# Optimization experiments

Measured on AMD Instinct MI355X. Metric: run time of the kernel, lower is better.

## Reference

```python
import jax, jax.numpy as jnp
import numpy as np

S, B, D, H = 512, 256, 256, 256  # seq, batch, input_dim, hidden_dim
E = D + H                        # attention embed dim


def setup_inputs() -> dict:
    key = jax.random.key(0)
    ks = jax.random.split(key, 9)
    w = lambda k, shape: (jax.random.normal(k, shape, jnp.float32) * 0.02)
    return {
        "inputs": jax.random.normal(ks[0], (S, B, D), jnp.float32),
        "Wq": w(ks[1], (E, E)),
        "Wk": w(ks[2], (E, E)),
        "Wv": w(ks[3], (E, E)),
        "Wf": w(ks[4], (H, E)), "bf": jnp.zeros((H,), jnp.float32),
        "Wi": w(ks[5], (H, E)), "bi": jnp.zeros((H,), jnp.float32),
        "Wg": w(ks[6], (H, E)), "bg": jnp.zeros((H,), jnp.float32),
        "Wo": w(ks[7], (H, E)), "bo": jnp.zeros((H,), jnp.float32),
    }


def reference(inputs, Wq, Wk, Wv, Wf, bf, Wi, bi, Wg, bg, Wo, bo):
    seq, batch, d_in = inputs.shape
    h_dim = Wf.shape[0]
    scale = 1.0 / np.sqrt(d_in + h_dim)

    def step(carry, x):
        hx, cx = carry
        comb = jnp.concatenate([x, hx], axis=1)            # (B, E)
        q = comb @ Wq.T
        k = comb @ Wk.T
        v = comb @ Wv.T
        # NOTE: attention is over the batch dimension, as in the source.
        scores = jax.nn.softmax((q @ k.T) * scale, axis=-1)  # (B, B)
        attn = scores @ v                                    # (B, E)
        f = jax.nn.sigmoid(attn @ Wf.T + bf)
        i = jax.nn.sigmoid(attn @ Wi.T + bi)
        g = jnp.tanh(attn @ Wg.T + bg)
        o = jax.nn.sigmoid(attn @ Wo.T + bo)
        cx_new = f * cx + i * g
        hx_new = o * jnp.tanh(cx_new)
        return (hx_new, cx_new), hx_new

    init = (jnp.zeros((batch, h_dim), inputs.dtype),
            jnp.zeros((batch, h_dim), inputs.dtype))
    (hx, cx), stacked = jax.lax.scan(step, init, inputs)
    return stacked, (hx, cx)
```

## Files before the change

### kernel.cpp

```cpp
#include <hip/hip_runtime.h>
#include <hip/hip_bf16.h>


typedef __hip_bfloat16 bf16;
typedef __attribute__((ext_vector_type(8))) short bf16x8;
typedef __attribute__((ext_vector_type(4))) float f32x4;
typedef unsigned long long u64;

#define SEQ 512
#define NSTEP 8
#define BB  256
#define DD  256
#define HH  256
#define EE  512
#define NWG 64
#define QK_SCALE 0.04419417382415922f

#define WS_COMB0  0
#define WS_COMB1  262144
#define WS_COMBT0 524288
#define WS_COMBT1 786432
#define WS_CX     1048576
#define WS_MT     1310720
#define WS_UF     1835008
#define WS_UI     2097152
#define WS_UG     2359296
#define WS_UO     2621440
#define WS_FLAGS  2883584
#define WS_REL    2887680
#define WS_END    2888192

__device__ __forceinline__ float sigm(float x) { return 1.0f / (1.0f + __expf(-x)); }

__device__ __forceinline__ unsigned short f2bf_s(float f) {
  bf16 h = __float2bfloat16(f);
  return *reinterpret_cast<unsigned short*>(&h);
}
__device__ __forceinline__ u64 pack4(float a, float b, float c, float d) {
  union { unsigned short s[4]; u64 u; } x;
  x.s[0] = f2bf_s(a); x.s[1] = f2bf_s(b); x.s[2] = f2bf_s(c); x.s[3] = f2bf_s(d);
  return x.u;
}
__device__ __forceinline__ void sta8(void* p, u64 v) {
  __hip_atomic_store((u64*)p, v, __ATOMIC_RELAXED, __HIP_MEMORY_SCOPE_AGENT);
}
__device__ __forceinline__ unsigned lda4(const unsigned* p) {
  return __hip_atomic_load(p, __ATOMIC_RELAXED, __HIP_MEMORY_SCOPE_AGENT);
}
__device__ __forceinline__ void sta4(unsigned* p, unsigned v) {
  __hip_atomic_store(p, v, __ATOMIC_RELAXED, __HIP_MEMORY_SCOPE_AGENT);
}
#define LOAD16_COH(dst, addr) \
  asm volatile("global_load_dwordx4 %0, %1, off sc0 sc1" : "=v"(dst) : "v"(addr))

__device__ __forceinline__ void gbar64(unsigned* flags, unsigned* rel,
                                       int wg, unsigned val) {
  asm volatile("s_waitcnt vmcnt(0)" ::: "memory");
  __syncthreads();
  const int tid = threadIdx.x;
  if (wg == NWG - 1) {
    if (tid < 64) {
      if (tid == 0) sta4(&flags[(NWG - 1) * 16], val);
      if (tid < NWG) {
        while (lda4(&flags[tid * 16]) < val) __builtin_amdgcn_s_sleep(1);
      }
    }
    __syncthreads();
    if (tid < 8) sta4(&rel[tid * 16], val);
  } else {
    if (tid == 0) {
      sta4(&flags[wg * 16], val);
      while (lda4(&rel[(wg & 7) * 16]) < val) __builtin_amdgcn_s_sleep(1);
    }
  }
  __syncthreads();
}

__global__ void __launch_bounds__(256) qlstm_init_kernel(
    const float* __restrict__ x,
    const float* __restrict__ Wq, const float* __restrict__ Wk, const float* __restrict__ Wv,
    const float* __restrict__ Wf, const float* __restrict__ Wi,
    const float* __restrict__ Wg, const float* __restrict__ Wo,
    char* __restrict__ wsb)
{
  const int gid = blockIdx.x * blockDim.x + threadIdx.x;
  bf16* comb0  = (bf16*)(wsb + WS_COMB0);
  bf16* combT0 = (bf16*)(wsb + WS_COMBT0);
  float* cx    = (float*)(wsb + WS_CX);
  bf16* mt     = (bf16*)(wsb + WS_MT);

  if (gid < 65536) {
    const int i = gid >> 8, e = gid & 255;
    const bf16 xv = __float2bfloat16(x[i * DD + e]);
    comb0[i * EE + e] = xv;
    comb0[i * EE + 256 + e] = __float2bfloat16(0.0f);
    combT0[e * BB + i] = xv;
    combT0[(256 + e) * BB + i] = __float2bfloat16(0.0f);
  } else {
    cx[gid - 65536] = 0.0f;
  }
  if (gid < (WS_END - WS_FLAGS) / 4) ((unsigned*)(wsb + WS_FLAGS))[gid] = 0u;

  #pragma unroll 1
  for (int kk = 0; kk < 2; ++kk) {
    const int o = gid + kk * 131072;
    const int n = o >> 9, e = o & 511;
    float acc = 0.0f;
    #pragma unroll 4
    for (int j = 0; j < 512; ++j) acc = __builtin_fmaf(Wq[j * 512 + e], Wk[j * 512 + n], acc);
    mt[o] = __float2bfloat16(acc);
  }
  const float* srcs[4] = { Wf, Wi, Wg, Wo };
  const int offs[4] = { WS_UF, WS_UI, WS_UG, WS_UO };
  #pragma unroll 1
  for (int a = 0; a < 4; ++a) {
    bf16* U = (bf16*)(wsb + offs[a]);
    const float* W = srcs[a];
    const int h = gid >> 9, e = gid & 511;
    float acc = 0.0f;
    #pragma unroll 4
    for (int ep = 0; ep < 512; ++ep) acc = __builtin_fmaf(W[h * 512 + ep], Wv[ep * 512 + e], acc);
    U[gid] = __float2bfloat16(acc);
  }
}

__global__ void __launch_bounds__(1024) qlstm_step_kernel(
    const float* __restrict__ x,
    const float* __restrict__ bfv, const float* __restrict__ biv,
    const float* __restrict__ bgv, const float* __restrict__ bov,
    float* __restrict__ out, char* __restrict__ wsb, int t0, int bbase)
{
  float* cx_ws = (float*)(wsb + WS_CX);
  const bf16* mt   = (const bf16*)(wsb + WS_MT);
  const bf16* uf_b = (const bf16*)(wsb + WS_UF);
  const bf16* ui_b = (const bf16*)(wsb + WS_UI);
  const bf16* ug_b = (const bf16*)(wsb + WS_UG);
  const bf16* uo_b = (const bf16*)(wsb + WS_UO);
  unsigned* flags = (unsigned*)(wsb + WS_FLAGS);
  unsigned* rel   = (unsigned*)(wsb + WS_REL);

  const int wg   = blockIdx.x;
  const int s    = wg >> 2;
  const int q4   = wg & 3;
  const int r0   = s * 16;
  const int tid  = threadIdx.x;
  const int wid  = tid >> 6;
  const int lane = tid & 63;
  const int l16  = lane & 15;
  const int kq   = lane >> 4;

  __shared__ unsigned short c_lds[16 * 520];
  __shared__ unsigned short z_lds[16 * 520];
  __shared__ unsigned short a_lds[16 * 520];
  __shared__ float          s_lds[16 * 256];
  __shared__ unsigned short p_lds[16 * 264];
  __shared__ float          g_lds[16 * 256];
  __shared__ unsigned short ht_lds[64 * 18];

  for (int k = 0; k < NSTEP; ++k) {
    const int t = t0 + k;
    const int par = t & 1;
    const bf16* comb   = (const bf16*)(wsb + (par ? WS_COMB1 : WS_COMB0));
    const bf16* combT  = (const bf16*)(wsb + (par ? WS_COMBT1 : WS_COMBT0));
    bf16* combN  = (bf16*)(wsb + (par ? WS_COMB0 : WS_COMB1));
    bf16* combTN = (bf16*)(wsb + (par ? WS_COMBT0 : WS_COMBT1));

    {
      const int row = tid >> 6, c8 = (tid & 63) * 8;
      bf16x8 cv;
      LOAD16_COH(cv, comb + (size_t)(r0 + row) * EE + c8);
      asm volatile("s_waitcnt vmcnt(0)" ::: "memory");
      *(bf16x8*)(&c_lds[row * 520 + c8]) = cv;
    }
    __syncthreads();

    #pragma unroll
    for (int h2 = 0; h2 < 2; ++h2) {
      const int n0 = (wid * 2 + h2) * 16;
      const bf16* arow = mt + (size_t)(n0 + l16) * EE;
      const unsigned short* brow = &c_lds[l16 * 520];
      f32x4 acc = {0.f, 0.f, 0.f, 0.f};
      #pragma unroll
      for (int half = 0; half < 2; ++half) {
        bf16x8 mfr[8];
        #pragma unroll
        for (int u = 0; u < 8; ++u)
          mfr[u] = *(const bf16x8*)(arow + (half * 8 + u) * 32 + kq * 8);
        #pragma unroll
        for (int u = 0; u < 8; ++u) {
          bf16x8 bf8 = *(const bf16x8*)(brow + (half * 8 + u) * 32 + kq * 8);
          acc = __builtin_amdgcn_mfma_f32_16x16x32_bf16(mfr[u], bf8, acc, 0, 0, 0);
        }
      }
      *(u64*)(&z_lds[l16 * 520 + n0 + kq * 4]) = pack4(acc[0], acc[1], acc[2], acc[3]);
    }
    __syncthreads();
    {
      const int j0 = wid * 16;
      const unsigned short* arow = &z_lds[l16 * 520];
      const bf16* brow = comb + (size_t)(j0 + l16) * EE;
      f32x4 acc = {0.f, 0.f, 0.f, 0.f};
      #pragma unroll
      for (int half = 0; half < 2; ++half) {
        bf16x8 cfr[8];
        #pragma unroll
        for (int u = 0; u < 8; ++u)
          LOAD16_COH(cfr[u], brow + (half * 8 + u) * 32 + kq * 8);
        asm volatile("s_waitcnt vmcnt(0)" ::: "memory");
        __builtin_amdgcn_sched_barrier(0);
        #pragma unroll
        for (int u = 0; u < 8; ++u) {
          bf16x8 af = *(const bf16x8*)(arow + (half * 8 + u) * 32 + kq * 8);
          acc = __builtin_amdgcn_mfma_f32_16x16x32_bf16(af, cfr[u], acc, 0, 0, 0);
        }
      }
      #pragma unroll
      for (int r = 0; r < 4; ++r)
        s_lds[(kq * 4 + r) * 256 + j0 + l16] = acc[r];
    }
    __syncthreads();
    {
      const int i = wid;
      const float4 v = *(const float4*)(&s_lds[i * 256 + lane * 4]);
      float m = fmaxf(fmaxf(v.x, v.y), fmaxf(v.z, v.w));
      #pragma unroll
      for (int off = 32; off > 0; off >>= 1) m = fmaxf(m, __shfl_xor(m, off));
      float e0 = __expf((v.x - m) * QK_SCALE);
      float e1 = __expf((v.y - m) * QK_SCALE);
      float e2 = __expf((v.z - m) * QK_SCALE);
      float e3 = __expf((v.w - m) * QK_SCALE);
      float sum = e0 + e1 + e2 + e3;
      #pragma unroll
      for (int off = 32; off > 0; off >>= 1) sum += __shfl_xor(sum, off);
      const float rinv = 1.0f / sum;
      unsigned short* pp = &p_lds[i * 264 + lane * 4];
      pp[0] = f2bf_s(e0 * rinv);
      pp[1] = f2bf_s(e1 * rinv);
      pp[2] = f2bf_s(e2 * rinv);
      pp[3] = f2bf_s(e3 * rinv);
    }
    __syncthreads();
    #pragma unroll
    for (int q8 = 0; q8 < 2; ++q8) {
      const int n0 = wid * 16 + q8 * 256;
      const bf16* arow = combT + (size_t)(n0 + l16) * BB;
      const unsigned short* brow = &p_lds[l16 * 264];
      f32x4 acc = {0.f, 0.f, 0.f, 0.f};
      bf16x8 tfr[8];
      #pragma unroll
      for (int u = 0; u < 8; ++u)
        LOAD16_COH(tfr[u], arow + u * 32 + kq * 8);
      asm volatile("s_waitcnt vmcnt(0)" ::: "memory");
      __builtin_amdgcn_sched_barrier(0);
      #pragma unroll
      for (int u = 0; u < 8; ++u) {
        bf16x8 bf8 = *(const bf16x8*)(brow + u * 32 + kq * 8);
        acc = __builtin_amdgcn_mfma_f32_16x16x32_bf16(tfr[u], bf8, acc, 0, 0, 0);
      }
      *(u64*)(&a_lds[l16 * 520 + n0 + kq * 4]) = pack4(acc[0], acc[1], acc[2], acc[3]);
    }
    __syncthreads();
    {
      const int g   = wid >> 2;
      const int hcb = wid & 3;
      const int h0  = q4 * 64 + hcb * 16;
      const bf16* U = (g == 0) ? uf_b : (g == 1) ? ui_b : (g == 2) ? ug_b : uo_b;
      const unsigned short* arow = &a_lds[l16 * 520];
      const bf16* brow = U + (size_t)(h0 + l16) * EE;
      f32x4 acc = {0.f, 0.f, 0.f, 0.f};
      #pragma unroll
      for (int half = 0; half < 2; ++half) {
        bf16x8 ufr[8];
        #pragma unroll
        for (int u = 0; u < 8; ++u)
          ufr[u] = *(const bf16x8*)(brow + (half * 8 + u) * 32 + kq * 8);
        #pragma unroll
        for (int u = 0; u < 8; ++u) {
          bf16x8 af = *(const bf16x8*)(arow + (half * 8 + u) * 32 + kq * 8);
          acc = __builtin_amdgcn_mfma_f32_16x16x32_bf16(af, ufr[u], acc, 0, 0, 0);
        }
      }
      #pragma unroll
      for (int r = 0; r < 4; ++r)
        g_lds[wid * 256 + (kq * 4 + r) * 16 + l16] = acc[r];
    }
    __syncthreads();
    {
      const int hcb2 = tid >> 8;
      const int idx  = tid & 255;
      const int i    = idx >> 4, c = idx & 15;
      const int colg = q4 * 64 + hcb2 * 16 + c;
      const float F = sigm(g_lds[(0 * 4 + hcb2) * 256 + idx] + bfv[colg]);
      const float I = sigm(g_lds[(1 * 4 + hcb2) * 256 + idx] + biv[colg]);
      const float G = tanhf(g_lds[(2 * 4 + hcb2) * 256 + idx] + bgv[colg]);
      const float O = sigm(g_lds[(3 * 4 + hcb2) * 256 + idx] + bov[colg]);
      float* cxp = cx_ws + (size_t)wg * 1024 + tid;
      const float c2 = F * (*cxp) + I * G;
      const float h  = O * tanhf(c2);
      *cxp = c2;
      out[(size_t)t * 65536 + (size_t)(r0 + i) * 256 + colg] = h;
      if (t < SEQ - 1) {
        const bf16 hb = __float2bfloat16(h);
        ht_lds[(hcb2 * 16 + c) * 18 + i] = *reinterpret_cast<const unsigned short*>(&hb);
      } else {
        out[(size_t)SEQ * 65536 + (size_t)(r0 + i) * 256 + colg] = h;
        out[(size_t)SEQ * 65536 + 65536 + (size_t)(r0 + i) * 256 + colg] = c2;
      }
    }
    __syncthreads();
    if (t < SEQ - 1) {
      if (tid < 256) {
        const int i = tid >> 4, c4 = (tid & 15) * 4;
        union { unsigned short sv[4]; u64 u; } pk;
        #pragma unroll
        for (int j = 0; j < 4; ++j) pk.sv[j] = ht_lds[(c4 + j) * 18 + i];
        sta8(combN + (size_t)(r0 + i) * EE + 256 + q4 * 64 + c4, pk.u);
      }
      if (tid < 128) {
        const int row64 = tid >> 1, half = tid & 1;
        const int e = 256 + q4 * 64 + row64;
        sta8(combTN + (size_t)e * BB + r0 + half * 8,
             *(const u64*)(&ht_lds[row64 * 18 + half * 8]));
        sta8(combTN + (size_t)e * BB + r0 + half * 8 + 4,
             *(const u64*)(&ht_lds[row64 * 18 + half * 8 + 4]));
      }
      if (q4 == 0) {
        unsigned short* xT = c_lds;
        {
          const int i2 = tid >> 6, e4 = (tid & 63) * 4;
          const float4 xf = *(const float4*)(x + ((size_t)(t + 1) * BB + r0 + i2) * DD + e4);
          const u64 p = pack4(xf.x, xf.y, xf.z, xf.w);
          const unsigned short* ps = (const unsigned short*)&p;
          xT[(e4 + 0) * 18 + i2] = ps[0];
          xT[(e4 + 1) * 18 + i2] = ps[1];
          xT[(e4 + 2) * 18 + i2] = ps[2];
          xT[(e4 + 3) * 18 + i2] = ps[3];
          sta8(combN + (size_t)(r0 + i2) * EE + e4, p);
        }
        __syncthreads();
        if (tid < 512) {
          const int row = tid >> 1, half = tid & 1;
          sta8(combTN + (size_t)row * BB + r0 + half * 8,
               *(const u64*)(&xT[row * 18 + half * 8]));
          sta8(combTN + (size_t)row * BB + r0 + half * 8 + 4,
               *(const u64*)(&xT[row * 18 + half * 8 + 4]));
        }
      }
    }
    if (k < NSTEP - 1) gbar64(flags, rel, wg, (unsigned)(bbase + k + 1));
  }
}

extern "C" void kernel_launch(void* const* d_in, const int* in_sizes, int n_in,
                              void* d_out, int out_size, void* d_ws, size_t ws_size,
                              hipStream_t stream) {
  const float* x   = (const float*)d_in[0];
  const float* Wq  = (const float*)d_in[1];
  const float* Wk  = (const float*)d_in[2];
  const float* Wv  = (const float*)d_in[3];
  const float* Wf  = (const float*)d_in[4];
  const float* bfv = (const float*)d_in[5];
  const float* Wi  = (const float*)d_in[6];
  const float* biv = (const float*)d_in[7];
  const float* Wgg = (const float*)d_in[8];
  const float* bgv = (const float*)d_in[9];
  const float* Wo  = (const float*)d_in[10];
  const float* bov = (const float*)d_in[11];
  float* out = (float*)d_out;
  char* wsb = (char*)d_ws;

  hipLaunchKernelGGL(qlstm_init_kernel, dim3(512), dim3(256), 0, stream,
                     x, Wq, Wk, Wv, Wf, Wi, Wgg, Wo, wsb);

  for (int d = 0; d < SEQ / NSTEP; ++d) {
    int t0 = d * NSTEP;
    int bbase = d * (NSTEP - 1);
    hipLaunchKernelGGL(qlstm_step_kernel, dim3(NWG), dim3(1024), 0, stream,
                       x, bfv, biv, bgv, bov, out, wsb, t0, bbase);
  }
}
```

Measured before the change: 21.14 ms.

## Run whole sequence in one cooperative kernel with 16 workgroups

Replaces the 64 launches of 8 steps each with a single cooperative launch of 16 workgroups that loops over all timesteps. Each workgroup now owns a 16-row batch slice and handles all four 64-column hidden chunks itself, so the flat 16-way barrier replaces the two-level 64-way barrier. The first GEMM reads comb directly from global memory into registers instead of staging it through LDS. This cuts launch overhead and grid-sync cost, but leaves 4x less parallelism per step, so each workgroup does more serial work on the gate GEMM and cell update.

Result: slower. 38.53 ms (+82.3%).

```diff
diff --git a/kernel.cpp b/kernel.cpp
--- a/kernel.cpp
+++ b/kernel.cpp
@@ -8,12 +8,11 @@
 typedef unsigned long long u64;
 
 #define SEQ 512
-#define NSTEP 8
 #define BB  256
 #define DD  256
 #define HH  256
 #define EE  512
-#define NWG 64
+#define NWG 16
 #define QK_SCALE 0.04419417382415922f
 
 #define WS_COMB0  0
@@ -27,8 +26,7 @@
 #define WS_UG     2359296
 #define WS_UO     2621440
 #define WS_FLAGS  2883584
-#define WS_REL    2887680
-#define WS_END    2888192
+#define WS_END    2884608
 
 __device__ __forceinline__ float sigm(float x) { return 1.0f / (1.0f + __expf(-x)); }
 
@@ -53,25 +51,12 @@
 #define LOAD16_COH(dst, addr) \
   asm volatile("global_load_dwordx4 %0, %1, off sc0 sc1" : "=v"(dst) : "v"(addr))
 
-__device__ __forceinline__ void gbar64(unsigned* flags, unsigned* rel,
-                                       int wg, unsigned val) {
+__device__ __forceinline__ void gbar16(unsigned* flags, int wg, unsigned val) {
   asm volatile("s_waitcnt vmcnt(0)" ::: "memory");
   __syncthreads();
-  const int tid = threadIdx.x;
-  if (wg == NWG - 1) {
-    if (tid < 64) {
-      if (tid == 0) sta4(&flags[(NWG - 1) * 16], val);
-      if (tid < NWG) {
-        while (lda4(&flags[tid * 16]) < val) __builtin_amdgcn_s_sleep(1);
-      }
-    }
-    __syncthreads();
-    if (tid < 8) sta4(&rel[tid * 16], val);
-  } else {
-    if (tid == 0) {
-      sta4(&flags[wg * 16], val);
-      while (lda4(&rel[(wg & 7) * 16]) < val) __builtin_amdgcn_s_sleep(1);
-    }
+  if (threadIdx.x == 0) sta4(&flags[wg * 16], val);
+  if (threadIdx.x < 16) {
+    while (lda4(&flags[threadIdx.x * 16]) < val) __builtin_amdgcn_s_sleep(1);
   }
   __syncthreads();
 }
@@ -124,11 +109,11 @@
   }
 }
 
-__global__ void __launch_bounds__(1024) qlstm_step_kernel(
+__global__ void __launch_bounds__(1024, 1) qlstm_main_kernel(
     const float* __restrict__ x,
     const float* __restrict__ bfv, const float* __restrict__ biv,
     const float* __restrict__ bgv, const float* __restrict__ bov,
-    float* __restrict__ out, char* __restrict__ wsb, int t0, int bbase)
+    float* __restrict__ out, char* __restrict__ wsb)
 {
   float* cx_ws = (float*)(wsb + WS_CX);
   const bf16* mt   = (const bf16*)(wsb + WS_MT);
@@ -137,19 +122,15 @@
   const bf16* ug_b = (const bf16*)(wsb + WS_UG);
   const bf16* uo_b = (const bf16*)(wsb + WS_UO);
   unsigned* flags = (unsigned*)(wsb + WS_FLAGS);
-  unsigned* rel   = (unsigned*)(wsb + WS_REL);
 
   const int wg   = blockIdx.x;
-  const int s    = wg >> 2;
-  const int q4   = wg & 3;
-  const int r0   = s * 16;
+  const int r0   = wg * 16;
   const int tid  = threadIdx.x;
   const int wid  = tid >> 6;
   const int lane = tid & 63;
   const int l16  = lane & 15;
   const int kq   = lane >> 4;
 
-  __shared__ unsigned short c_lds[16 * 520];
   __shared__ unsigned short z_lds[16 * 520];
   __shared__ unsigned short a_lds[16 * 520];
   __shared__ float          s_lds[16 * 256];
@@ -157,8 +138,7 @@
   __shared__ float          g_lds[16 * 256];
   __shared__ unsigned short ht_lds[64 * 18];
 
-  for (int k = 0; k < NSTEP; ++k) {
-    const int t = t0 + k;
+  for (int t = 0; t < SEQ; ++t) {
     const int par = t & 1;
     const bf16* comb   = (const bf16*)(wsb + (par ? WS_COMB1 : WS_COMB0));
     const bf16* combT  = (const bf16*)(wsb + (par ? WS_COMBT1 : WS_COMBT0));
@@ -166,33 +146,33 @@
     bf16* combTN = (bf16*)(wsb + (par ? WS_COMBT0 : WS_COMBT1));
 
     {
-      const int row = tid >> 6, c8 = (tid & 63) * 8;
-      bf16x8 cv;
-      LOAD16_COH(cv, comb + (size_t)(r0 + row) * EE + c8);
-      asm volatile("s_waitcnt vmcnt(0)" ::: "memory");
-      *(bf16x8*)(&c_lds[row * 520 + c8]) = cv;
-    }
-    __syncthreads();
-
-    #pragma unroll
-    for (int h2 = 0; h2 < 2; ++h2) {
-      const int n0 = (wid * 2 + h2) * 16;
-      const bf16* arow = mt + (size_t)(n0 + l16) * EE;
-      const unsigned short* brow = &c_lds[l16 * 520];
-      f32x4 acc = {0.f, 0.f, 0.f, 0.f};
+      const bf16* mrow0 = mt + (size_t)(wid * 32 + l16) * EE;
+      const bf16* mrow1 = mt + (size_t)(wid * 32 + 16 + l16) * EE;
+      const bf16* crow  = comb + (size_t)(r0 + l16) * EE;
+      f32x4 acc0 = {0.f, 0.f, 0.f, 0.f}, acc1 = {0.f, 0.f, 0.f, 0.f};
       #pragma unroll
       for (int half = 0; half < 2; ++half) {
-        bf16x8 mfr[8];
-        #pragma unroll
-        for (int u = 0; u < 8; ++u)
-          mfr[u] = *(const bf16x8*)(arow + (half * 8 + u) * 32 + kq * 8);
-        #pragma unroll
-        for (int u = 0; u < 8; ++u) {
-          bf16x8 bf8 = *(const bf16x8*)(brow + (half * 8 + u) * 32 + kq * 8);
-          acc = __builtin_amdgcn_mfma_f32_16x16x32_bf16(mfr[u], bf8, acc, 0, 0, 0);
-        }
-      }
-      *(u64*)(&z_lds[l16 * 520 + n0 + kq * 4]) = pack4(acc[0], acc[1], acc[2], acc[3]);
+        bf16x8 cfr[8], mfr[8];
+        #pragma unroll
+        for (int u = 0; u < 8; ++u)
+          LOAD16_COH(cfr[u], crow + (half * 8 + u) * 32 + kq * 8);
+        #pragma unroll
+        for (int u = 0; u < 8; ++u)
+          mfr[u] = *(const bf16x8*)(mrow0 + (half * 8 + u) * 32 + kq * 8);
+        asm volatile("s_waitcnt vmcnt(0)" ::: "memory");
+        __builtin_amdgcn_sched_barrier(0);
+        #pragma unroll
+        for (int u = 0; u < 8; ++u)
+          acc0 = __builtin_amdgcn_mfma_f32_16x16x32_bf16(mfr[u], cfr[u], acc0, 0, 0, 0);
+        #pragma unroll
+        for (int u = 0; u < 8; ++u)
+          mfr[u] = *(const bf16x8*)(mrow1 + (half * 8 + u) * 32 + kq * 8);
+        #pragma unroll
+        for (int u = 0; u < 8; ++u)
+          acc1 = __builtin_amdgcn_mfma_f32_16x16x32_bf16(mfr[u], cfr[u], acc1, 0, 0, 0);
+      }
+      *(u64*)(&z_lds[l16 * 520 + wid * 32 + kq * 4]) = pack4(acc0[0], acc0[1], acc0[2], acc0[3]);
+      *(u64*)(&z_lds[l16 * 520 + wid * 32 + 16 + kq * 4]) = pack4(acc1[0], acc1[1], acc1[2], acc1[3]);
     }
     __syncthreads();
     {
@@ -260,94 +240,97 @@
       *(u64*)(&a_lds[l16 * 520 + n0 + kq * 4]) = pack4(acc[0], acc[1], acc[2], acc[3]);
     }
     __syncthreads();
-    {
-      const int g   = wid >> 2;
-      const int hcb = wid & 3;
-      const int h0  = q4 * 64 + hcb * 16;
-      const bf16* U = (g == 0) ? uf_b : (g == 1) ? ui_b : (g == 2) ? ug_b : uo_b;
-      const unsigned short* arow = &a_lds[l16 * 520];
-      const bf16* brow = U + (size_t)(h0 + l16) * EE;
-      f32x4 acc = {0.f, 0.f, 0.f, 0.f};
-      #pragma unroll
-      for (int half = 0; half < 2; ++half) {
-        bf16x8 ufr[8];
-        #pragma unroll
-        for (int u = 0; u < 8; ++u)
-          ufr[u] = *(const bf16x8*)(brow + (half * 8 + u) * 32 + kq * 8);
-        #pragma unroll
-        for (int u = 0; u < 8; ++u) {
-          bf16x8 af = *(const bf16x8*)(arow + (half * 8 + u) * 32 + kq * 8);
-          acc = __builtin_amdgcn_mfma_f32_16x16x32_bf16(af, ufr[u], acc, 0, 0, 0);
-        }
-      }
-      #pragma unroll
-      for (int r = 0; r < 4; ++r)
-        g_lds[wid * 256 + (kq * 4 + r) * 16 + l16] = acc[r];
-    }
-    __syncthreads();
-    {
-      const int hcb2 = tid >> 8;
-      const int idx  = tid & 255;
-      const int i    = idx >> 4, c = idx & 15;
-      const int colg = q4 * 64 + hcb2 * 16 + c;
-      const float F = sigm(g_lds[(0 * 4 + hcb2) * 256 + idx] + bfv[colg]);
-      const float I = sigm(g_lds[(1 * 4 + hcb2) * 256 + idx] + biv[colg]);
-      const float G = tanhf(g_lds[(2 * 4 + hcb2) * 256 + idx] + bgv[colg]);
-      const float O = sigm(g_lds[(3 * 4 + hcb2) * 256 + idx] + bov[colg]);
-      float* cxp = cx_ws + (size_t)wg * 1024 + tid;
-      const float c2 = F * (*cxp) + I * G;
-      const float h  = O * tanhf(c2);
-      *cxp = c2;
-      out[(size_t)t * 65536 + (size_t)(r0 + i) * 256 + colg] = h;
+    #pragma unroll 1
+    for (int er = 0; er < 4; ++er) {
+      {
+        const int g   = wid >> 2;
+        const int hcb = er * 4 + (wid & 3);
+        const int h0  = hcb * 16;
+        const bf16* U = (g == 0) ? uf_b : (g == 1) ? ui_b : (g == 2) ? ug_b : uo_b;
+        const unsigned short* arow = &a_lds[l16 * 520];
+        const bf16* brow = U + (size_t)(h0 + l16) * EE;
+        f32x4 acc = {0.f, 0.f, 0.f, 0.f};
+        #pragma unroll
+        for (int half = 0; half < 2; ++half) {
+          bf16x8 ufr[8];
+          #pragma unroll
+          for (int u = 0; u < 8; ++u)
+            ufr[u] = *(const bf16x8*)(brow + (half * 8 + u) * 32 + kq * 8);
+          #pragma unroll
+          for (int u = 0; u < 8; ++u) {
+            bf16x8 af = *(const bf16x8*)(arow + (half * 8 + u) * 32 + kq * 8);
+            acc = __builtin_amdgcn_mfma_f32_16x16x32_bf16(af, ufr[u], acc, 0, 0, 0);
+          }
+        }
+        #pragma unroll
+        for (int r = 0; r < 4; ++r)
+          g_lds[wid * 256 + (kq * 4 + r) * 16 + l16] = acc[r];
+      }
+      __syncthreads();
+      {
+        const int hcb2 = tid >> 8;
+        const int idx  = tid & 255;
+        const int i    = idx >> 4, c = idx & 15;
+        const int colg = er * 64 + hcb2 * 16 + c;
+        const float F = sigm(g_lds[(0 * 4 + hcb2) * 256 + idx] + bfv[colg]);
+        const float I = sigm(g_lds[(1 * 4 + hcb2) * 256 + idx] + biv[colg]);
+        const float G = tanhf(g_lds[(2 * 4 + hcb2) * 256 + idx] + bgv[colg]);
+        const float O = sigm(g_lds[(3 * 4 + hcb2) * 256 + idx] + bov[colg]);
+        float* cxp = cx_ws + ((size_t)(wg * 4 + er) * 1024) + tid;
+        const float c2 = F * (*cxp) + I * G;
+        const float h  = O * tanhf(c2);
+        *cxp = c2;
+        out[(size_t)t * 65536 + (size_t)(r0 + i) * 256 + colg] = h;
+        if (t < SEQ - 1) {
+          const bf16 hb = __float2bfloat16(h);
+          ht_lds[(hcb2 * 16 + c) * 18 + i] = *reinterpret_cast<const unsigned short*>(&hb);
+        } else {
+          out[(size_t)SEQ * 65536 + (size_t)(r0 + i) * 256 + colg] = h;
+          out[(size_t)SEQ * 65536 + 65536 + (size_t)(r0 + i) * 256 + colg] = c2;
+        }
+      }
+      __syncthreads();
       if (t < SEQ - 1) {
-        const bf16 hb = __float2bfloat16(h);
-        ht_lds[(hcb2 * 16 + c) * 18 + i] = *reinterpret_cast<const unsigned short*>(&hb);
-      } else {
-        out[(size_t)SEQ * 65536 + (size_t)(r0 + i) * 256 + colg] = h;
-        out[(size_t)SEQ * 65536 + 65536 + (size_t)(r0 + i) * 256 + colg] = c2;
-      }
-    }
-    __syncthreads();
+        if (tid < 256) {
+          const int i = tid >> 4, c4 = (tid & 15) * 4;
+          union { unsigned short sv[4]; u64 u; } pk;
+          #pragma unroll
+          for (int j = 0; j < 4; ++j) pk.sv[j] = ht_lds[(c4 + j) * 18 + i];
+          sta8(combN + (size_t)(r0 + i) * EE + 256 + er * 64 + c4, pk.u);
+        }
+        if (tid < 128) {
+          const int row64 = tid >> 1, half = tid & 1;
+          const int e = 256 + er * 64 + row64;
+          sta8(combTN + (size_t)e * BB + r0 + half * 8,
+               *(const u64*)(&ht_lds[row64 * 18 + half * 8]));
+          sta8(combTN + (size_t)e * BB + r0 + half * 8 + 4,
+               *(const u64*)(&ht_lds[row64 * 18 + half * 8 + 4]));
+        }
+      }
+    }
     if (t < SEQ - 1) {
-      if (tid < 256) {
-        const int i = tid >> 4, c4 = (tid & 15) * 4;
-        union { unsigned short sv[4]; u64 u; } pk;
-        #pragma unroll
-        for (int j = 0; j < 4; ++j) pk.sv[j] = ht_lds[(c4 + j) * 18 + i];
-        sta8(combN + (size_t)(r0 + i) * EE + 256 + q4 * 64 + c4, pk.u);
-      }
-      if (tid < 128) {
-        const int row64 = tid >> 1, half = tid & 1;
-        const int e = 256 + q4 * 64 + row64;
-        sta8(combTN + (size_t)e * BB + r0 + half * 8,
-             *(const u64*)(&ht_lds[row64 * 18 + half * 8]));
-        sta8(combTN + (size_t)e * BB + r0 + half * 8 + 4,
-             *(const u64*)(&ht_lds[row64 * 18 + half * 8 + 4]));
-      }
-      if (q4 == 0) {
-        unsigned short* xT = c_lds;
-        {
-          const int i2 = tid >> 6, e4 = (tid & 63) * 4;
-          const float4 xf = *(const float4*)(x + ((size_t)(t + 1) * BB + r0 + i2) * DD + e4);
-          const u64 p = pack4(xf.x, xf.y, xf.z, xf.w);
-          const unsigned short* ps = (const unsigned short*)&p;
-          xT[(e4 + 0) * 18 + i2] = ps[0];
-          xT[(e4 + 1) * 18 + i2] = ps[1];
-          xT[(e4 + 2) * 18 + i2] = ps[2];
-          xT[(e4 + 3) * 18 + i2] = ps[3];
-          sta8(combN + (size_t)(r0 + i2) * EE + e4, p);
-        }
-        __syncthreads();
-        if (tid < 512) {
-          const int row = tid >> 1, half = tid & 1;
-          sta8(combTN + (size_t)row * BB + r0 + half * 8,
-               *(const u64*)(&xT[row * 18 + half * 8]));
-          sta8(combTN + (size_t)row * BB + r0 + half * 8 + 4,
-               *(const u64*)(&xT[row * 18 + half * 8 + 4]));
-        }
-      }
-    }
-    if (k < NSTEP - 1) gbar64(flags, rel, wg, (unsigned)(bbase + k + 1));
+      unsigned short* xT = z_lds;
+      {
+        const int i2 = tid >> 6, e4 = (tid & 63) * 4;
+        const float4 xf = *(const float4*)(x + ((size_t)(t + 1) * BB + r0 + i2) * DD + e4);
+        const u64 p = pack4(xf.x, xf.y, xf.z, xf.w);
+        const unsigned short* ps = (const unsigned short*)&p;
+        xT[(e4 + 0) * 18 + i2] = ps[0];
+        xT[(e4 + 1) * 18 + i2] = ps[1];
+        xT[(e4 + 2) * 18 + i2] = ps[2];
+        xT[(e4 + 3) * 18 + i2] = ps[3];
+        sta8(combN + (size_t)(r0 + i2) * EE + e4, p);
+      }
+      __syncthreads();
+      if (tid < 512) {
+        const int row = tid >> 1, half = tid & 1;
+        sta8(combTN + (size_t)row * BB + r0 + half * 8,
+             *(const u64*)(&xT[row * 18 + half * 8]));
+        sta8(combTN + (size_t)row * BB + r0 + half * 8 + 4,
+             *(const u64*)(&xT[row * 18 + half * 8 + 4]));
+      }
+      gbar16(flags, wg, (unsigned)(t + 1));
+    }
   }
 }
 
@@ -372,10 +355,8 @@
   hipLaunchKernelGGL(qlstm_init_kernel, dim3(512), dim3(256), 0, stream,
                      x, Wq, Wk, Wv, Wf, Wi, Wgg, Wo, wsb);
 
-  for (int d = 0; d < SEQ / NSTEP; ++d) {
-    int t0 = d * NSTEP;
-    int bbase = d * (NSTEP - 1);
-    hipLaunchKernelGGL(qlstm_step_kernel, dim3(NWG), dim3(1024), 0, stream,
-                       x, bfv, biv, bgv, bov, out, wsb, t0, bbase);
-  }
-}
+  void* args[] = { (void*)&x, (void*)&bfv, (void*)&biv, (void*)&bgv, (void*)&bov,
+                   (void*)&out, (void*)&wsb };
+  hipLaunchCooperativeKernel((void*)qlstm_main_kernel, dim3(NWG), dim3(1024),
+                             args, 0, stream);
+}
```

## Split comb into h and x buffers, precompute transposed x for all steps

Applied to the files above, without the earlier changes.

The combined [x|h] buffers and their transposes become separate h, hT and xT buffers. The x part of each step's input is now read straight from the fp32 input and converted in-kernel, so per-step writes of x into comb go away. When the workspace is large enough, a separate kernel precomputes transposed bf16 x for every timestep, which removes the per-step transpose done by q4==0 workgroups before the grid barrier. This costs an extra 64MB of workspace and one extra kernel launch, and keeps a fallback path for smaller workspaces.

Result: slower. 24.31 ms (+15.0%).

```diff
diff --git a/kernel.cpp b/kernel.cpp
--- a/kernel.cpp
+++ b/kernel.cpp
@@ -16,19 +16,23 @@
 #define NWG 64
 #define QK_SCALE 0.04419417382415922f
 
-#define WS_COMB0  0
-#define WS_COMB1  262144
-#define WS_COMBT0 524288
-#define WS_COMBT1 786432
-#define WS_CX     1048576
-#define WS_MT     1310720
-#define WS_UF     1835008
-#define WS_UI     2097152
-#define WS_UG     2359296
-#define WS_UO     2621440
-#define WS_FLAGS  2883584
-#define WS_REL    2887680
-#define WS_END    2888192
+#define WS_H0     0
+#define WS_H1     131072
+#define WS_HT0    262144
+#define WS_HT1    393216
+#define WS_XT0    524288
+#define WS_XT1    655360
+#define WS_CX     786432
+#define WS_MT     1048576
+#define WS_UF     1572864
+#define WS_UI     1835008
+#define WS_UG     2097152
+#define WS_UO     2359296
+#define WS_FLAGS  2621440
+#define WS_REL    2625536
+#define WS_END    2626048
+#define WS_XTALL  2626048
+#define WS_NEED_XTALL (WS_XTALL + 67108864ull)
 
 __device__ __forceinline__ float sigm(float x) { return 1.0f / (1.0f + __expf(-x)); }
 
@@ -40,6 +44,14 @@
   union { unsigned short s[4]; u64 u; } x;
   x.s[0] = f2bf_s(a); x.s[1] = f2bf_s(b); x.s[2] = f2bf_s(c); x.s[3] = f2bf_s(d);
   return x.u;
+}
+__device__ __forceinline__ bf16x8 cvt8(float4 a, float4 b) {
+  bf16x8 r;
+  r[0] = (short)f2bf_s(a.x); r[1] = (short)f2bf_s(a.y);
+  r[2] = (short)f2bf_s(a.z); r[3] = (short)f2bf_s(a.w);
+  r[4] = (short)f2bf_s(b.x); r[5] = (short)f2bf_s(b.y);
+  r[6] = (short)f2bf_s(b.z); r[7] = (short)f2bf_s(b.w);
+  return r;
 }
 __device__ __forceinline__ void sta8(void* p, u64 v) {
   __hip_atomic_store((u64*)p, v, __ATOMIC_RELAXED, __HIP_MEMORY_SCOPE_AGENT);
@@ -84,18 +96,16 @@
     char* __restrict__ wsb)
 {
   const int gid = blockIdx.x * blockDim.x + threadIdx.x;
-  bf16* comb0  = (bf16*)(wsb + WS_COMB0);
-  bf16* combT0 = (bf16*)(wsb + WS_COMBT0);
-  float* cx    = (float*)(wsb + WS_CX);
-  bf16* mt     = (bf16*)(wsb + WS_MT);
+  bf16* h0  = (bf16*)(wsb + WS_H0);
+  bf16* ht0 = (bf16*)(wsb + WS_HT0);
+  bf16* xt0 = (bf16*)(wsb + WS_XT0);
+  float* cx = (float*)(wsb + WS_CX);
+  bf16* mt  = (bf16*)(wsb + WS_MT);
 
   if (gid < 65536) {
-    const int i = gid >> 8, e = gid & 255;
-    const bf16 xv = __float2bfloat16(x[i * DD + e]);
-    comb0[i * EE + e] = xv;
-    comb0[i * EE + 256 + e] = __float2bfloat16(0.0f);
-    combT0[e * BB + i] = xv;
-    combT0[(256 + e) * BB + i] = __float2bfloat16(0.0f);
+    h0[gid]  = __float2bfloat16(0.0f);
+    ht0[gid] = __float2bfloat16(0.0f);
+    xt0[gid] = __float2bfloat16(x[(size_t)(gid & 255) * DD + (gid >> 8)]);
   } else {
     cx[gid - 65536] = 0.0f;
   }
@@ -124,11 +134,48 @@
   }
 }
 
+__global__ void __launch_bounds__(256) qlstm_xt_kernel(
+    const float* __restrict__ x, char* __restrict__ wsb)
+{
+  bf16* xt_all = (bf16*)(wsb + WS_XTALL);
+  const int bid = blockIdx.x;
+  const int t  = bid >> 2;
+  const int eb = bid & 3;
+  const int tid = threadIdx.x;
+  __shared__ unsigned short lds[64 * 72];
+
+  #pragma unroll 1
+  for (int ic = 0; ic < 4; ++ic) {
+    #pragma unroll
+    for (int sub = 0; sub < 4; ++sub) {
+      const int i_loc = tid >> 4;
+      const int e4    = (tid & 15) * 4;
+      const int row   = ic * 64 + sub * 16 + i_loc;
+      const float4 v = *(const float4*)(x + ((size_t)t * BB + row) * DD + eb * 64 + e4);
+      const int il = sub * 16 + i_loc;
+      lds[(e4 + 0) * 72 + il] = f2bf_s(v.x);
+      lds[(e4 + 1) * 72 + il] = f2bf_s(v.y);
+      lds[(e4 + 2) * 72 + il] = f2bf_s(v.z);
+      lds[(e4 + 3) * 72 + il] = f2bf_s(v.w);
+    }
+    __syncthreads();
+    #pragma unroll
+    for (int half = 0; half < 2; ++half) {
+      const int e  = half * 32 + (tid >> 3);
+      const int i8 = (tid & 7) * 8;
+      *(bf16x8*)(xt_all + (size_t)t * 65536 + (size_t)(eb * 64 + e) * 256 + ic * 64 + i8) =
+          *(const bf16x8*)(&lds[e * 72 + i8]);
+    }
+    __syncthreads();
+  }
+}
+
 __global__ void __launch_bounds__(1024) qlstm_step_kernel(
     const float* __restrict__ x,
     const float* __restrict__ bfv, const float* __restrict__ biv,
     const float* __restrict__ bgv, const float* __restrict__ bov,
-    float* __restrict__ out, char* __restrict__ wsb, int t0, int bbase)
+    float* __restrict__ out, char* __restrict__ wsb, int t0, int bbase,
+    int use_xtall)
 {
   float* cx_ws = (float*)(wsb + WS_CX);
   const bf16* mt   = (const bf16*)(wsb + WS_MT);
@@ -136,6 +183,7 @@
   const bf16* ui_b = (const bf16*)(wsb + WS_UI);
   const bf16* ug_b = (const bf16*)(wsb + WS_UG);
   const bf16* uo_b = (const bf16*)(wsb + WS_UO);
+  const bf16* xt_all = (const bf16*)(wsb + WS_XTALL);
   unsigned* flags = (unsigned*)(wsb + WS_FLAGS);
   unsigned* rel   = (unsigned*)(wsb + WS_REL);
 
@@ -160,16 +208,24 @@
   for (int k = 0; k < NSTEP; ++k) {
     const int t = t0 + k;
     const int par = t & 1;
-    const bf16* comb   = (const bf16*)(wsb + (par ? WS_COMB1 : WS_COMB0));
-    const bf16* combT  = (const bf16*)(wsb + (par ? WS_COMBT1 : WS_COMBT0));
-    bf16* combN  = (bf16*)(wsb + (par ? WS_COMB0 : WS_COMB1));
-    bf16* combTN = (bf16*)(wsb + (par ? WS_COMBT0 : WS_COMBT1));
+    const bf16* h_cur   = (const bf16*)(wsb + (par ? WS_H1  : WS_H0));
+    const bf16* ht_cur  = (const bf16*)(wsb + (par ? WS_HT1 : WS_HT0));
+    const bf16* xt_cur  = use_xtall ? (xt_all + ((size_t)t << 16))
+                                    : (const bf16*)(wsb + (par ? WS_XT1 : WS_XT0));
+    bf16* h_nxt  = (bf16*)(wsb + (par ? WS_H0  : WS_H1));
+    bf16* ht_nxt = (bf16*)(wsb + (par ? WS_HT0 : WS_HT1));
+    bf16* xt_nxt = (bf16*)(wsb + (par ? WS_XT0 : WS_XT1));
 
     {
       const int row = tid >> 6, c8 = (tid & 63) * 8;
       bf16x8 cv;
-      LOAD16_COH(cv, comb + (size_t)(r0 + row) * EE + c8);
-      asm volatile("s_waitcnt vmcnt(0)" ::: "memory");
+      if (c8 < 256) {
+        const float4* xf = (const float4*)(x + ((size_t)t * BB + r0 + row) * DD + c8);
+        cv = cvt8(xf[0], xf[1]);
+      } else {
+        LOAD16_COH(cv, h_cur + (size_t)(r0 + row) * HH + (c8 - 256));
+        asm volatile("s_waitcnt vmcnt(0)" ::: "memory");
+      }
       *(bf16x8*)(&c_lds[row * 520 + c8]) = cv;
     }
     __syncthreads();
@@ -198,19 +254,32 @@
     {
       const int j0 = wid * 16;
       const unsigned short* arow = &z_lds[l16 * 520];
-      const bf16* brow = comb + (size_t)(j0 + l16) * EE;
+      const float* xrow = x + ((size_t)t * BB + j0 + l16) * DD;
+      const bf16*  hrow = h_cur + (size_t)(j0 + l16) * HH;
       f32x4 acc = {0.f, 0.f, 0.f, 0.f};
-      #pragma unroll
-      for (int half = 0; half < 2; ++half) {
+      {
         bf16x8 cfr[8];
         #pragma unroll
+        for (int u = 0; u < 8; ++u) {
+          const float4* xf = (const float4*)(xrow + u * 32 + kq * 8);
+          cfr[u] = cvt8(xf[0], xf[1]);
+        }
+        #pragma unroll
+        for (int u = 0; u < 8; ++u) {
+          bf16x8 af = *(const bf16x8*)(arow + u * 32 + kq * 8);
+          acc = __builtin_amdgcn_mfma_f32_16x16x32_bf16(af, cfr[u], acc, 0, 0, 0);
+        }
+      }
+      {
+        bf16x8 cfr[8];
+        #pragma unroll
         for (int u = 0; u < 8; ++u)
-          LOAD16_COH(cfr[u], brow + (half * 8 + u) * 32 + kq * 8);
+          LOAD16_COH(cfr[u], hrow + u * 32 + kq * 8);
         asm volatile("s_waitcnt vmcnt(0)" ::: "memory");
         __builtin_amdgcn_sched_barrier(0);
         #pragma unroll
         for (int u = 0; u < 8; ++u) {
-          bf16x8 af = *(const bf16x8*)(arow + (half * 8 + u) * 32 + kq * 8);
+          bf16x8 af = *(const bf16x8*)(arow + (8 + u) * 32 + kq * 8);
           acc = __builtin_amdgcn_mfma_f32_16x16x32_bf16(af, cfr[u], acc, 0, 0, 0);
         }
       }
@@ -240,24 +309,48 @@
       pp[3] = f2bf_s(e3 * rinv);
     }
     __syncthreads();
-    #pragma unroll
-    for (int q8 = 0; q8 < 2; ++q8) {
-      const int n0 = wid * 16 + q8 * 256;
-      const bf16* arow = combT + (size_t)(n0 + l16) * BB;
+    {
       const unsigned short* brow = &p_lds[l16 * 264];
-      f32x4 acc = {0.f, 0.f, 0.f, 0.f};
-      bf16x8 tfr[8];
-      #pragma unroll
-      for (int u = 0; u < 8; ++u)
-        LOAD16_COH(tfr[u], arow + u * 32 + kq * 8);
-      asm volatile("s_waitcnt vmcnt(0)" ::: "memory");
-      __builtin_amdgcn_sched_barrier(0);
-      #pragma unroll
-      for (int u = 0; u < 8; ++u) {
-        bf16x8 bf8 = *(const bf16x8*)(brow + u * 32 + kq * 8);
-        acc = __builtin_amdgcn_mfma_f32_16x16x32_bf16(tfr[u], bf8, acc, 0, 0, 0);
-      }
-      *(u64*)(&a_lds[l16 * 520 + n0 + kq * 4]) = pack4(acc[0], acc[1], acc[2], acc[3]);
+      {
+        const int n0 = wid * 16;
+        const bf16* arow = xt_cur + (size_t)(n0 + l16) * BB;
+        f32x4 acc = {0.f, 0.f, 0.f, 0.f};
+        bf16x8 tfr[8];
+        if (use_xtall) {
+          #pragma unroll
+          for (int u = 0; u < 8; ++u)
+            tfr[u] = *(const bf16x8*)(arow + u * 32 + kq * 8);
+        } else {
+          #pragma unroll
+          for (int u = 0; u < 8; ++u)
+            LOAD16_COH(tfr[u], arow + u * 32 + kq * 8);
+          asm volatile("s_waitcnt vmcnt(0)" ::: "memory");
+          __builtin_amdgcn_sched_barrier(0);
+        }
+        #pragma unroll
+        for (int u = 0; u < 8; ++u) {
+          bf16x8 bf8 = *(const bf16x8*)(brow + u * 32 + kq * 8);
+          acc = __builtin_amdgcn_mfma_f32_16x16x32_bf16(tfr[u], bf8, acc, 0, 0, 0);
+        }
+        *(u64*)(&a_lds[l16 * 520 + n0 + kq * 4]) = pack4(acc[0], acc[1], acc[2], acc[3]);
+      }
+      {
+        const int n0 = wid * 16;
+        const bf16* arow = ht_cur + (size_t)(n0 + l16) * BB;
+        f32x4 acc = {0.f, 0.f, 0.f, 0.f};
+        bf16x8 tfr[8];
+        #pragma unroll
+        for (int u = 0; u < 8; ++u)
+          LOAD16_COH(tfr[u], arow + u * 32 + kq * 8);
+        asm volatile("s_waitcnt vmcnt(0)" ::: "memory");
+        __builtin_amdgcn_sched_barrier(0);
+        #pragma unroll
+        for (int u = 0; u < 8; ++u) {
+          bf16x8 bf8 = *(const bf16x8*)(brow + u * 32 + kq * 8);
+          acc = __builtin_amdgcn_mfma_f32_16x16x32_bf16(tfr[u], bf8, acc, 0, 0, 0);
+        }
+        *(u64*)(&a_lds[l16 * 520 + 256 + n0 + kq * 4]) = pack4(acc[0], acc[1], acc[2], acc[3]);
+      }
     }
     __syncthreads();
     {
@@ -314,17 +407,17 @@
         union { unsigned short sv[4]; u64 u; } pk;
         #pragma unroll
         for (int j = 0; j < 4; ++j) pk.sv[j] = ht_lds[(c4 + j) * 18 + i];
-        sta8(combN + (size_t)(r0 + i) * EE + 256 + q4 * 64 + c4, pk.u);
+        sta8(h_nxt + (size_t)(r0 + i) * HH + q4 * 64 + c4, pk.u);
       }
       if (tid < 128) {
         const int row64 = tid >> 1, half = tid & 1;
-        const int e = 256 + q4 * 64 + row64;
-        sta8(combTN + (size_t)e * BB + r0 + half * 8,
+        const int e = q4 * 64 + row64;
+        sta8(ht_nxt + (size_t)e * BB + r0 + half * 8,
              *(const u64*)(&ht_lds[row64 * 18 + half * 8]));
-        sta8(combTN + (size_t)e * BB + r0 + half * 8 + 4,
+        sta8(ht_nxt + (size_t)e * BB + r0 + half * 8 + 4,
              *(const u64*)(&ht_lds[row64 * 18 + half * 8 + 4]));
       }
-      if (q4 == 0) {
+      if (!use_xtall && q4 == 0) {
         unsigned short* xT = c_lds;
         {
           const int i2 = tid >> 6, e4 = (tid & 63) * 4;
@@ -335,14 +428,13 @@
           xT[(e4 + 1) * 18 + i2] = ps[1];
           xT[(e4 + 2) * 18 + i2] = ps[2];
           xT[(e4 + 3) * 18 + i2] = ps[3];
-          sta8(combN + (size_t)(r0 + i2) * EE + e4, p);
         }
         __syncthreads();
         if (tid < 512) {
           const int row = tid >> 1, half = tid & 1;
-          sta8(combTN + (size_t)row * BB + r0 + half * 8,
+          sta8(xt_nxt + (size_t)row * BB + r0 + half * 8,
                *(const u64*)(&xT[row * 18 + half * 8]));
-          sta8(combTN + (size_t)row * BB + r0 + half * 8 + 4,
+          sta8(xt_nxt + (size_t)row * BB + r0 + half * 8 + 4,
                *(const u64*)(&xT[row * 18 + half * 8 + 4]));
         }
       }
@@ -369,13 +461,18 @@
   float* out = (float*)d_out;
   char* wsb = (char*)d_ws;
 
+  const int use_xtall = (ws_size >= WS_NEED_XTALL) ? 1 : 0;
+
   hipLaunchKernelGGL(qlstm_init_kernel, dim3(512), dim3(256), 0, stream,
                      x, Wq, Wk, Wv, Wf, Wi, Wgg, Wo, wsb);
+  if (use_xtall) {
+    hipLaunchKernelGGL(qlstm_xt_kernel, dim3(2048), dim3(256), 0, stream, x, wsb);
+  }
 
   for (int d = 0; d < SEQ / NSTEP; ++d) {
     int t0 = d * NSTEP;
     int bbase = d * (NSTEP - 1);
     hipLaunchKernelGGL(qlstm_step_kernel, dim3(NWG), dim3(1024), 0, stream,
-                       x, bfv, biv, bgv, bov, out, wsb, t0, bbase);
-  }
-}
+                       x, bfv, biv, bgv, bov, out, wsb, t0, bbase, use_xtall);
+  }
+}
```
